# Performance work log

Measured on AMD Instinct MI355X. Metric: run time of the kernel, lower is better.

The kernel has to match this reference:

```python
import jax, jax.numpy as jnp
import numpy as np
import math

B, T, VOCAB, RANK = 32, 1024, 512, 256


def setup_inputs() -> dict:
    key = jax.random.key(0)
    k1, k2, k3, k4, k5 = jax.random.split(key, 5)
    scale_attn = 1.0 / math.sqrt(VOCAB)
    scale_proj = 1.0 / math.sqrt(RANK)
    return {
        "x": jax.random.normal(k1, (B, T, VOCAB), dtype=jnp.float32),
        "W_attn": jax.random.normal(k2, (VOCAB, 3 * RANK), dtype=jnp.float32) * scale_attn,
        "b_attn": jax.random.normal(k3, (3 * RANK,), dtype=jnp.float32) * 0.01,
        "W_proj": jax.random.normal(k4, (RANK, VOCAB), dtype=jnp.float32) * scale_proj,
        "b_proj": jax.random.normal(k5, (VOCAB,), dtype=jnp.float32) * 0.01,
    }


def reference(x, W_attn, b_attn, W_proj, b_proj):
    # x: [B, T, vocab]
    Bb, Tt, _ = x.shape
    qkv = x @ W_attn + b_attn              # [B, T, 3*rank]
    q, k, v = jnp.split(qkv, 3, axis=-1)   # each [B, T, rank]
    scale = 1.0 / math.sqrt(k.shape[-1])
    att = jnp.einsum('btd,bsd->bts', q, k) * scale  # [B, T, T]
    # causal mask (masked=True)
    mask = jnp.tril(jnp.ones((Tt, Tt), dtype=bool))
    att = jnp.where(mask[None, :, :], att, -jnp.inf)
    att = jax.nn.softmax(att, axis=-1)
    # dropout layers are identity in eval mode (p=0 attn, p=0.1 resid disabled)
    y = jnp.einsum('bts,bsd->btd', att, v)  # [B, T, rank]
    y = y @ W_proj + b_proj                 # [B, T, vocab]
    return jax.nn.gelu(y, approximate=False)
```

## Files before the change

### kernel.cpp

```cpp
#include <hip/hip_runtime.h>
#include <hip/hip_bf16.h>
#include <math.h>

typedef __bf16 bf16;
typedef __attribute__((ext_vector_type(8))) __bf16 bf16x8;
typedef __attribute__((ext_vector_type(4))) __bf16 bf16x4;
typedef __attribute__((ext_vector_type(4))) float f32x4;

#define MFMA16(a, b, c) __builtin_amdgcn_mfma_f32_16x16x32_bf16((a), (b), (c), 0, 0, 0)


__global__ __launch_bounds__(256) void cvt_wattn(const float* __restrict__ w,
                                                 bf16* __restrict__ wt) {
  int o = blockIdx.x * 256 + threadIdx.x;
  int n = o >> 9, kk = o & 511;
  wt[o] = (bf16)w[kk * 768 + n];
}

__global__ __launch_bounds__(256) void cvt_wproj(const float* __restrict__ w,
                                                 bf16* __restrict__ wt) {
  int o = blockIdx.x * 256 + threadIdx.x;
  int n = o >> 8, kk = o & 255;
  wt[o] = (bf16)w[kk * 512 + n];
}

__global__ __launch_bounds__(256) void gemm_qkv(
    const float* __restrict__ x, const bf16* __restrict__ WT,
    const float* __restrict__ b_attn,
    bf16* __restrict__ qo, bf16* __restrict__ ko, bf16* __restrict__ vo) {
  __shared__ __attribute__((aligned(16))) bf16 As[128][40];
  __shared__ __attribute__((aligned(16))) bf16 Bs[128][40];
  const int tid = threadIdx.x;
  const int id = blockIdx.x;
  const int xcd = id & 7;
  const int rest = id >> 3;
  const int bmL = rest / 6;
  const int bn = (rest % 6) * 128;
  const int bm = (xcd * 32 + bmL) * 128;
  const int lane = tid & 63, wid = tid >> 6;
  const int l15 = lane & 15, lg = lane >> 4;
  const int wm = (wid >> 1) * 64, wn = (wid & 1) * 64;

  f32x4 acc[4][4] = {};

  const int srow = tid >> 1;
  const int scol = (tid & 1) * 16;
  const float* xp = x + (size_t)(bm + srow) * 512 + scol;
  const bf16* wp = WT + (size_t)(bn + srow) * 512 + scol;

  bf16x8 ha[2], hb[2];
  {
    f32x4 f0 = *(const f32x4*)(xp);
    f32x4 f1 = *(const f32x4*)(xp + 4);
    f32x4 f2 = *(const f32x4*)(xp + 8);
    f32x4 f3 = *(const f32x4*)(xp + 12);
#pragma unroll
    for (int e = 0; e < 4; ++e) {
      ha[0][e] = (bf16)f0[e]; ha[0][e + 4] = (bf16)f1[e];
      ha[1][e] = (bf16)f2[e]; ha[1][e + 4] = (bf16)f3[e];
    }
    hb[0] = *(const bf16x8*)(wp);
    hb[1] = *(const bf16x8*)(wp + 8);
  }

  for (int kt = 0; kt < 16; ++kt) {
    __syncthreads();
    *(bf16x8*)&As[srow][scol] = ha[0];
    *(bf16x8*)&As[srow][scol + 8] = ha[1];
    *(bf16x8*)&Bs[srow][scol] = hb[0];
    *(bf16x8*)&Bs[srow][scol + 8] = hb[1];
    __syncthreads();
    if (kt < 15) {
      f32x4 f0 = *(const f32x4*)(xp + (kt + 1) * 32);
      f32x4 f1 = *(const f32x4*)(xp + (kt + 1) * 32 + 4);
      f32x4 f2 = *(const f32x4*)(xp + (kt + 1) * 32 + 8);
      f32x4 f3 = *(const f32x4*)(xp + (kt + 1) * 32 + 12);
#pragma unroll
      for (int e = 0; e < 4; ++e) {
        ha[0][e] = (bf16)f0[e]; ha[0][e + 4] = (bf16)f1[e];
        ha[1][e] = (bf16)f2[e]; ha[1][e + 4] = (bf16)f3[e];
      }
      hb[0] = *(const bf16x8*)(wp + (kt + 1) * 32);
      hb[1] = *(const bf16x8*)(wp + (kt + 1) * 32 + 8);
    }
    bf16x8 af[4], bfr[4];
#pragma unroll
    for (int mi = 0; mi < 4; ++mi)
      af[mi] = *(const bf16x8*)&As[wm + mi * 16 + l15][lg * 8];
#pragma unroll
    for (int ni = 0; ni < 4; ++ni)
      bfr[ni] = *(const bf16x8*)&Bs[wn + ni * 16 + l15][lg * 8];
    __builtin_amdgcn_s_setprio(1);
#pragma unroll
    for (int mi = 0; mi < 4; ++mi)
#pragma unroll
      for (int ni = 0; ni < 4; ++ni)
        acc[mi][ni] = MFMA16(af[mi], bfr[ni], acc[mi][ni]);
    __builtin_amdgcn_s_setprio(0);
  }

#pragma unroll
  for (int ni = 0; ni < 4; ++ni) {
    int gc = bn + wn + ni * 16 + l15;
    float bias = b_attn[gc];
    int seg = gc >> 8;
    int cc = gc & 255;
    bf16* op = (seg == 0) ? qo : ((seg == 1) ? ko : vo);
#pragma unroll
    for (int mi = 0; mi < 4; ++mi) {
      int gr = bm + wm + mi * 16 + lg * 4;
#pragma unroll
      for (int r = 0; r < 4; ++r) {
        float v = acc[mi][ni][r] + bias;
        op[(size_t)(gr + r) * 256 + cc] = (bf16)v;
      }
    }
  }
}

__global__ __launch_bounds__(256) void transpose_v(const bf16* __restrict__ v,
                                                   bf16* __restrict__ vt) {
  __shared__ bf16 tile[32][33];
  const int b = blockIdx.z;
  const int t0 = blockIdx.x * 32;
  const int d0 = blockIdx.y * 32;
  const int tid = threadIdx.x;
  const int r = tid >> 3, c4 = (tid & 7) * 4;
  bf16x4 in = *(const bf16x4*)(v + (size_t)(b * 1024 + t0 + r) * 256 + d0 + c4);
  tile[r][c4] = in[0]; tile[r][c4 + 1] = in[1];
  tile[r][c4 + 2] = in[2]; tile[r][c4 + 3] = in[3];
  __syncthreads();
  bf16x4 o;
  o[0] = tile[c4][r]; o[1] = tile[c4 + 1][r];
  o[2] = tile[c4 + 2][r]; o[3] = tile[c4 + 3][r];
  *(bf16x4*)(vt + (size_t)(b * 256 + d0 + r) * 1024 + t0 + c4) = o;
}

__global__ __launch_bounds__(512) void attn_fwd(
    const bf16* __restrict__ q, const bf16* __restrict__ k,
    const bf16* __restrict__ vt, bf16* __restrict__ y) {
  __shared__ __attribute__((aligned(16))) bf16 Ks[64][264];
  __shared__ __attribute__((aligned(16))) bf16 Vt[256][72];
  __shared__ __attribute__((aligned(16))) bf16 Ps[8][16][72];
  const int tid = threadIdx.x, lane = tid & 63, wid = tid >> 6;
  const int l15 = lane & 15, lg = lane >> 4;

  const int id = blockIdx.x;
  const int xcd = id & 7;
  const int rest = id >> 3;
  const int qt = rest & 7;
  const int bg = rest >> 3;
  const int b = xcd + 8 * bg;
  const int q0 = qt * 128 + wid * 16;

  bf16x8 qf[8];
  {
    const bf16* qp = q + (size_t)(b * 1024 + q0 + l15) * 256 + lg * 8;
#pragma unroll
    for (int d = 0; d < 8; ++d) qf[d] = *(const bf16x8*)(qp + d * 32);
  }
  f32x4 o[16] = {};
  float m_st = -1e30f;
  float l_st = 0.f;

  const bf16* kbase = k + (size_t)b * 1024 * 256;
  const bf16* vtbase = vt + (size_t)b * 256 * 1024;
  const int ksr = tid >> 5, ksc = (tid & 31) * 8;
  const int vsr = tid >> 3, vsc = (tid & 7) * 8;

  const int ntiles = 2 * qt + 2;

  bf16x8 kreg[4], vreg[4];
#pragma unroll
  for (int i = 0; i < 4; ++i)
    kreg[i] = *(const bf16x8*)(kbase + (size_t)(ksr + i * 16) * 256 + ksc);
#pragma unroll
  for (int i = 0; i < 4; ++i)
    vreg[i] = *(const bf16x8*)(vtbase + (size_t)(vsr + i * 64) * 1024 + vsc);

  for (int tt = 0; tt < ntiles; ++tt) {
    const int kv0 = tt * 64;
    __syncthreads();
#pragma unroll
    for (int i = 0; i < 4; ++i)
      *(bf16x8*)&Ks[ksr + i * 16][ksc] = kreg[i];
#pragma unroll
    for (int i = 0; i < 4; ++i)
      *(bf16x8*)&Vt[vsr + i * 64][vsc] = vreg[i];
    __syncthreads();
    if (tt + 1 < ntiles) {
      const bf16* kp = kbase + (size_t)(kv0 + 64 + ksr) * 256 + ksc;
      const bf16* vp = vtbase + (size_t)vsr * 1024 + kv0 + 64 + vsc;
#pragma unroll
      for (int i = 0; i < 4; ++i)
        kreg[i] = *(const bf16x8*)(kp + (size_t)i * 16 * 256);
#pragma unroll
      for (int i = 0; i < 4; ++i)
        vreg[i] = *(const bf16x8*)(vp + (size_t)i * 64 * 1024);
    }

    f32x4 st[4] = {};
    __builtin_amdgcn_s_setprio(1);
#pragma unroll
    for (int nf = 0; nf < 4; ++nf)
#pragma unroll
      for (int dc = 0; dc < 8; ++dc) {
        bf16x8 kb = *(const bf16x8*)&Ks[nf * 16 + l15][dc * 32 + lg * 8];
        st[nf] = MFMA16(kb, qf[dc], st[nf]);
      }
    __builtin_amdgcn_s_setprio(0);

    const int qg = q0 + l15;
    float tmax = -1e30f;
#pragma unroll
    for (int nf = 0; nf < 4; ++nf)
#pragma unroll
      for (int r = 0; r < 4; ++r) {
        int sg = kv0 + nf * 16 + lg * 4 + r;
        float v = st[nf][r] * 0.0625f;
        v = (sg > qg) ? -1e30f : v;
        st[nf][r] = v;
        tmax = fmaxf(tmax, v);
      }
    tmax = fmaxf(tmax, __shfl_xor(tmax, 16, 64));
    tmax = fmaxf(tmax, __shfl_xor(tmax, 32, 64));

    if (!__all(tmax <= m_st + 8.f)) {
      float mnew = fmaxf(m_st, tmax);
      float corr = __expf(m_st - mnew);
      m_st = mnew;
      l_st *= corr;
      float corrT[4];
#pragma unroll
      for (int r = 0; r < 4; ++r) corrT[r] = __shfl(corr, lg * 4 + r, 64);
#pragma unroll
      for (int df = 0; df < 16; ++df)
#pragma unroll
        for (int r = 0; r < 4; ++r) o[df][r] *= corrT[r];
    }

    float rsum = 0.f;
#pragma unroll
    for (int nf = 0; nf < 4; ++nf) {
      bf16x4 pk;
#pragma unroll
      for (int r = 0; r < 4; ++r) {
        float p = __expf(st[nf][r] - m_st);
        rsum += p;
        pk[r] = (bf16)p;
      }
      *(bf16x4*)&Ps[wid][l15][nf * 16 + lg * 4] = pk;
    }
    rsum += __shfl_xor(rsum, 16, 64);
    rsum += __shfl_xor(rsum, 32, 64);
    l_st += rsum;

    bf16x8 pa0 = *(const bf16x8*)&Ps[wid][l15][lg * 8];
    bf16x8 pa1 = *(const bf16x8*)&Ps[wid][l15][32 + lg * 8];
    __builtin_amdgcn_s_setprio(1);
#pragma unroll
    for (int df = 0; df < 16; ++df) {
      bf16x8 vb0 = *(const bf16x8*)&Vt[df * 16 + l15][lg * 8];
      bf16x8 vb1 = *(const bf16x8*)&Vt[df * 16 + l15][32 + lg * 8];
      o[df] = MFMA16(pa0, vb0, o[df]);
      o[df] = MFMA16(pa1, vb1, o[df]);
    }
    __builtin_amdgcn_s_setprio(0);
  }

  float lT[4];
#pragma unroll
  for (int r = 0; r < 4; ++r) lT[r] = __shfl(l_st, lg * 4 + r, 64);
  const size_t ybase = (size_t)(b * 1024 + q0 + lg * 4) * 256 + l15;
#pragma unroll
  for (int r = 0; r < 4; ++r) {
    float inv = 1.f / lT[r];
#pragma unroll
    for (int df = 0; df < 16; ++df)
      y[ybase + (size_t)r * 256 + df * 16] = (bf16)(o[df][r] * inv);
  }
}

__global__ __launch_bounds__(256) void gemm_proj(
    const bf16* __restrict__ y, const bf16* __restrict__ WT,
    const float* __restrict__ b_proj, float* __restrict__ out) {
  __shared__ __attribute__((aligned(16))) bf16 As[128][40];
  __shared__ __attribute__((aligned(16))) bf16 Bs[128][40];
  const int tid = threadIdx.x;
  const int bn = blockIdx.x * 128;
  const int bm = blockIdx.y * 128;
  const int lane = tid & 63, wid = tid >> 6;
  const int l15 = lane & 15, lg = lane >> 4;
  const int wm = (wid >> 1) * 64, wn = (wid & 1) * 64;
  f32x4 acc[4][4] = {};
  const int srow = tid >> 1, scol = (tid & 1) * 16;
  const bf16* yp = y + (size_t)(bm + srow) * 256 + scol;
  const bf16* wp = WT + (size_t)(bn + srow) * 256 + scol;
  for (int kt = 0; kt < 8; ++kt) {
    bf16x8 a0 = *(const bf16x8*)(yp + kt * 32);
    bf16x8 a1 = *(const bf16x8*)(yp + kt * 32 + 8);
    bf16x8 b0 = *(const bf16x8*)(wp + kt * 32);
    bf16x8 b1 = *(const bf16x8*)(wp + kt * 32 + 8);
    *(bf16x8*)&As[srow][scol] = a0;  *(bf16x8*)&As[srow][scol + 8] = a1;
    *(bf16x8*)&Bs[srow][scol] = b0;  *(bf16x8*)&Bs[srow][scol + 8] = b1;
    __syncthreads();
    bf16x8 af[4], bfr[4];
#pragma unroll
    for (int mi = 0; mi < 4; ++mi)
      af[mi] = *(const bf16x8*)&As[wm + mi * 16 + l15][lg * 8];
#pragma unroll
    for (int ni = 0; ni < 4; ++ni)
      bfr[ni] = *(const bf16x8*)&Bs[wn + ni * 16 + l15][lg * 8];
#pragma unroll
    for (int mi = 0; mi < 4; ++mi)
#pragma unroll
      for (int ni = 0; ni < 4; ++ni)
        acc[mi][ni] = MFMA16(af[mi], bfr[ni], acc[mi][ni]);
    __syncthreads();
  }
#pragma unroll
  for (int ni = 0; ni < 4; ++ni) {
    int gc = bn + wn + ni * 16 + l15;
    float bias = b_proj[gc];
#pragma unroll
    for (int mi = 0; mi < 4; ++mi) {
      int gr = bm + wm + mi * 16 + lg * 4;
#pragma unroll
      for (int r = 0; r < 4; ++r) {
        float v = acc[mi][ni][r] + bias;
        float g = 0.5f * v * (1.0f + erff(v * 0.70710678118654752f));
        out[(size_t)(gr + r) * 512 + gc] = g;
      }
    }
  }
}

extern "C" void kernel_launch(void* const* d_in, const int* in_sizes, int n_in,
                              void* d_out, int out_size, void* d_ws, size_t ws_size,
                              hipStream_t stream) {
  const float* x      = (const float*)d_in[0];
  const float* W_attn = (const float*)d_in[1];
  const float* b_attn = (const float*)d_in[2];
  const float* W_proj = (const float*)d_in[3];
  const float* b_proj = (const float*)d_in[4];
  float* out = (float*)d_out;
  char* ws = (char*)d_ws;

  const size_t SZ = 16777216;
  bf16* WT1 = (bf16*)(ws);
  bf16* WT2 = (bf16*)(ws + 786432);
  bf16* qb  = (bf16*)(ws + 1048576);
  bf16* kb  = (bf16*)(ws + 1048576 + SZ);
  bf16* vb  = (bf16*)(ws + 1048576 + 2 * SZ);
  bf16* vtb = (bf16*)(ws + 1048576 + 3 * SZ);
  bf16* yb  = vb;

  cvt_wattn<<<dim3(1536), dim3(256), 0, stream>>>(W_attn, WT1);
  cvt_wproj<<<dim3(512), dim3(256), 0, stream>>>(W_proj, WT2);
  gemm_qkv<<<dim3(1536), dim3(256), 0, stream>>>(x, WT1, b_attn, qb, kb, vb);
  transpose_v<<<dim3(32, 8, 32), dim3(256), 0, stream>>>(vb, vtb);
  attn_fwd<<<dim3(256), dim3(512), 0, stream>>>(qb, kb, vtb, yb);
  gemm_proj<<<dim3(4, 256), dim3(256), 0, stream>>>(yb, WT2, b_proj, out);
}
```

Measured before the change: 152.5 us.

## Pre-convert x to bf16 and load GEMM tiles via direct global-to-LDS

Adds a separate kernel that converts x to bf16 into workspace, so the QKV GEMM can stage A and B tiles with global_load_lds direct-to-LDS copies instead of register loads plus LDS stores. The LDS padding is removed to match the direct-load layout. The register prefetch double-buffering and setprio are dropped in favour of a simple load-sync-compute-sync loop. The projection GEMM uses the same load path and gets XCD-aware block swizzling. The cost is an extra full pass over x (read fp32, write bf16), the loss of load/compute overlap, and possible LDS bank conflicts on the now-unpadded rows.

```diff
diff --git a/kernel.cpp b/kernel.cpp
--- a/kernel.cpp
+++ b/kernel.cpp
@@ -8,6 +8,12 @@
 typedef __attribute__((ext_vector_type(4))) float f32x4;
 
 #define MFMA16(a, b, c) __builtin_amdgcn_mfma_f32_16x16x32_bf16((a), (b), (c), 0, 0, 0)
+
+__device__ __forceinline__ void glds16(const bf16* g, bf16* l) {
+  __builtin_amdgcn_global_load_lds(
+      (const __attribute__((address_space(1))) unsigned int*)g,
+      (__attribute__((address_space(3))) unsigned int*)l, 16, 0, 0);
+}
 
 
 __global__ __launch_bounds__(256) void cvt_wattn(const float* __restrict__ w,
@@ -24,12 +30,23 @@
   wt[o] = (bf16)w[kk * 512 + n];
 }
 
+__global__ __launch_bounds__(256) void cvt_x(const float* __restrict__ x,
+                                             bf16* __restrict__ xb) {
+  size_t i = ((size_t)blockIdx.x * 256 + threadIdx.x) * 8;
+  f32x4 f0 = *(const f32x4*)(x + i);
+  f32x4 f1 = *(const f32x4*)(x + i + 4);
+  bf16x8 h;
+#pragma unroll
+  for (int e = 0; e < 4; ++e) { h[e] = (bf16)f0[e]; h[e + 4] = (bf16)f1[e]; }
+  *(bf16x8*)(xb + i) = h;
+}
+
 __global__ __launch_bounds__(256) void gemm_qkv(
-    const float* __restrict__ x, const bf16* __restrict__ WT,
+    const bf16* __restrict__ xb, const bf16* __restrict__ WT,
     const float* __restrict__ b_attn,
     bf16* __restrict__ qo, bf16* __restrict__ ko, bf16* __restrict__ vo) {
-  __shared__ __attribute__((aligned(16))) bf16 As[128][40];
-  __shared__ __attribute__((aligned(16))) bf16 Bs[128][40];
+  __shared__ __attribute__((aligned(16))) bf16 As[128][32];
+  __shared__ __attribute__((aligned(16))) bf16 Bs[128][32];
   const int tid = threadIdx.x;
   const int id = blockIdx.x;
   const int xcd = id & 7;
@@ -43,46 +60,20 @@
 
   f32x4 acc[4][4] = {};
 
-  const int srow = tid >> 1;
-  const int scol = (tid & 1) * 16;
-  const float* xp = x + (size_t)(bm + srow) * 512 + scol;
-  const bf16* wp = WT + (size_t)(bn + srow) * 512 + scol;
-
-  bf16x8 ha[2], hb[2];
-  {
-    f32x4 f0 = *(const f32x4*)(xp);
-    f32x4 f1 = *(const f32x4*)(xp + 4);
-    f32x4 f2 = *(const f32x4*)(xp + 8);
-    f32x4 f3 = *(const f32x4*)(xp + 12);
-#pragma unroll
-    for (int e = 0; e < 4; ++e) {
-      ha[0][e] = (bf16)f0[e]; ha[0][e + 4] = (bf16)f1[e];
-      ha[1][e] = (bf16)f2[e]; ha[1][e + 4] = (bf16)f3[e];
-    }
-    hb[0] = *(const bf16x8*)(wp);
-    hb[1] = *(const bf16x8*)(wp + 8);
-  }
+  const int ar = tid >> 2;
+  const int ac = (tid & 3) * 8;
+  const bf16* aB = xb + (size_t)bm * 512 + (size_t)ar * 512 + ac;
+  const bf16* bB = WT + (size_t)bn * 512 + (size_t)ar * 512 + ac;
+  bf16* As0 = &As[0][0];
+  bf16* Bs0 = &Bs[0][0];
 
   for (int kt = 0; kt < 16; ++kt) {
-    __syncthreads();
-    *(bf16x8*)&As[srow][scol] = ha[0];
-    *(bf16x8*)&As[srow][scol + 8] = ha[1];
-    *(bf16x8*)&Bs[srow][scol] = hb[0];
-    *(bf16x8*)&Bs[srow][scol + 8] = hb[1];
-    __syncthreads();
-    if (kt < 15) {
-      f32x4 f0 = *(const f32x4*)(xp + (kt + 1) * 32);
-      f32x4 f1 = *(const f32x4*)(xp + (kt + 1) * 32 + 4);
-      f32x4 f2 = *(const f32x4*)(xp + (kt + 1) * 32 + 8);
-      f32x4 f3 = *(const f32x4*)(xp + (kt + 1) * 32 + 12);
-#pragma unroll
-      for (int e = 0; e < 4; ++e) {
-        ha[0][e] = (bf16)f0[e]; ha[0][e + 4] = (bf16)f1[e];
-        ha[1][e] = (bf16)f2[e]; ha[1][e + 4] = (bf16)f3[e];
-      }
-      hb[0] = *(const bf16x8*)(wp + (kt + 1) * 32);
-      hb[1] = *(const bf16x8*)(wp + (kt + 1) * 32 + 8);
-    }
+    const int k0 = kt * 32;
+    glds16(aB + k0,            As0 + (size_t)tid * 8);
+    glds16(aB + 64 * 512 + k0, As0 + (size_t)(256 + tid) * 8);
+    glds16(bB + k0,            Bs0 + (size_t)tid * 8);
+    glds16(bB + 64 * 512 + k0, Bs0 + (size_t)(256 + tid) * 8);
+    __syncthreads();
     bf16x8 af[4], bfr[4];
 #pragma unroll
     for (int mi = 0; mi < 4; ++mi)
@@ -90,13 +81,12 @@
 #pragma unroll
     for (int ni = 0; ni < 4; ++ni)
       bfr[ni] = *(const bf16x8*)&Bs[wn + ni * 16 + l15][lg * 8];
-    __builtin_amdgcn_s_setprio(1);
 #pragma unroll
     for (int mi = 0; mi < 4; ++mi)
 #pragma unroll
       for (int ni = 0; ni < 4; ++ni)
         acc[mi][ni] = MFMA16(af[mi], bfr[ni], acc[mi][ni]);
-    __builtin_amdgcn_s_setprio(0);
+    __syncthreads();
   }
 
 #pragma unroll
@@ -284,25 +274,33 @@
 __global__ __launch_bounds__(256) void gemm_proj(
     const bf16* __restrict__ y, const bf16* __restrict__ WT,
     const float* __restrict__ b_proj, float* __restrict__ out) {
-  __shared__ __attribute__((aligned(16))) bf16 As[128][40];
-  __shared__ __attribute__((aligned(16))) bf16 Bs[128][40];
+  __shared__ __attribute__((aligned(16))) bf16 As[128][32];
+  __shared__ __attribute__((aligned(16))) bf16 Bs[128][32];
   const int tid = threadIdx.x;
-  const int bn = blockIdx.x * 128;
-  const int bm = blockIdx.y * 128;
+  const int id = blockIdx.x;
+  const int xcd = id & 7;
+  const int rest = id >> 3;
+  const int bmL = rest >> 2;
+  const int bn = (rest & 3) * 128;
+  const int bm = (xcd * 32 + bmL) * 128;
   const int lane = tid & 63, wid = tid >> 6;
   const int l15 = lane & 15, lg = lane >> 4;
   const int wm = (wid >> 1) * 64, wn = (wid & 1) * 64;
   f32x4 acc[4][4] = {};
-  const int srow = tid >> 1, scol = (tid & 1) * 16;
-  const bf16* yp = y + (size_t)(bm + srow) * 256 + scol;
-  const bf16* wp = WT + (size_t)(bn + srow) * 256 + scol;
+
+  const int ar = tid >> 2;
+  const int ac = (tid & 3) * 8;
+  const bf16* aB = y + (size_t)bm * 256 + (size_t)ar * 256 + ac;
+  const bf16* bB = WT + (size_t)bn * 256 + (size_t)ar * 256 + ac;
+  bf16* As0 = &As[0][0];
+  bf16* Bs0 = &Bs[0][0];
+
   for (int kt = 0; kt < 8; ++kt) {
-    bf16x8 a0 = *(const bf16x8*)(yp + kt * 32);
-    bf16x8 a1 = *(const bf16x8*)(yp + kt * 32 + 8);
-    bf16x8 b0 = *(const bf16x8*)(wp + kt * 32);
-    bf16x8 b1 = *(const bf16x8*)(wp + kt * 32 + 8);
-    *(bf16x8*)&As[srow][scol] = a0;  *(bf16x8*)&As[srow][scol + 8] = a1;
-    *(bf16x8*)&Bs[srow][scol] = b0;  *(bf16x8*)&Bs[srow][scol + 8] = b1;
+    const int k0 = kt * 32;
+    glds16(aB + k0,            As0 + (size_t)tid * 8);
+    glds16(aB + 64 * 256 + k0, As0 + (size_t)(256 + tid) * 8);
+    glds16(bB + k0,            Bs0 + (size_t)tid * 8);
+    glds16(bB + 64 * 256 + k0, Bs0 + (size_t)(256 + tid) * 8);
     __syncthreads();
     bf16x8 af[4], bfr[4];
 #pragma unroll
@@ -354,11 +352,13 @@
   bf16* vb  = (bf16*)(ws + 1048576 + 2 * SZ);
   bf16* vtb = (bf16*)(ws + 1048576 + 3 * SZ);
   bf16* yb  = vb;
+  bf16* xbb = (bf16*)(ws + 1048576 + 3 * SZ);
 
   cvt_wattn<<<dim3(1536), dim3(256), 0, stream>>>(W_attn, WT1);
   cvt_wproj<<<dim3(512), dim3(256), 0, stream>>>(W_proj, WT2);
-  gemm_qkv<<<dim3(1536), dim3(256), 0, stream>>>(x, WT1, b_attn, qb, kb, vb);
+  cvt_x<<<dim3(8192), dim3(256), 0, stream>>>(x, xbb);
+  gemm_qkv<<<dim3(1536), dim3(256), 0, stream>>>(xbb, WT1, b_attn, qb, kb, vb);
   transpose_v<<<dim3(32, 8, 32), dim3(256), 0, stream>>>(vb, vtb);
   attn_fwd<<<dim3(256), dim3(512), 0, stream>>>(qb, kb, vtb, yb);
-  gemm_proj<<<dim3(4, 256), dim3(256), 0, stream>>>(yb, WT2, b_proj, out);
-}
+  gemm_proj<<<dim3(1024), dim3(256), 0, stream>>>(yb, WT2, b_proj, out);
+}
```

Measured after the change: 157.3 us. +3.1%, slower.
